# Kernel optimization log

Measured on AMD Instinct MI355X. Metric: run time of the kernel, lower is better.

## Reference

```python
import jax, jax.numpy as jnp
import numpy as np

B, S, F, E, H = 4, 2048, 512, 512, 8
DH = E // H


def setup_inputs() -> dict:
    key = jax.random.key(0)
    ks = jax.random.split(key, 8)
    sc = 1.0 / np.sqrt(F)
    return {
        "x": jax.random.normal(ks[0], (B, S, F), jnp.float32),
        "etype_emb": jax.random.normal(ks[1], (B, S, E), jnp.float32),
        "mask": jax.random.randint(ks[2], (B, S), 0, 2, jnp.int32),
        "Wq": jax.random.normal(ks[3], (F, E), jnp.float32) * sc,
        "bq": jnp.zeros((E,), jnp.float32),
        "Wk": jax.random.normal(ks[4], (F, E), jnp.float32) * sc,
        "bk": jnp.zeros((E,), jnp.float32),
        "Wv": jax.random.normal(ks[5], (F, E), jnp.float32) * sc,
        "bv": jnp.zeros((E,), jnp.float32),
    }


def _heads(t):
    # [B,S,E] -> [B,H,S,DH]; tf.split on last dim + concat on axis 1 == this reshape/transpose
    return t.reshape(B, S, H, DH).transpose(0, 2, 1, 3)


def reference(x, etype_emb, mask, Wq, bq, Wk, bk, Wv, bv):
    # Dropout is identity in inference mode (training=None)
    q = _heads(x @ Wq + bq + etype_emb)            # [B,H,S,DH]
    k = _heads(x @ Wk + bk)
    v = _heads(x @ Wv + bv)
    scores = jnp.einsum("bhqd,bhkd->bhqk", q, k) / jnp.sqrt(jnp.float32(DH))
    NEG = jnp.float32(-1e10)
    m = (mask == 1)
    # mask keys before softmax
    scores = jnp.where(m[:, None, None, :], scores, NEG)
    att = jax.nn.softmax(scores, axis=-1)
    # mask queries after softmax (zero out)
    att = jnp.where(m[:, None, :, None], att, jnp.float32(0.0))
    h = jnp.einsum("bhqk,bhkd->bhqd", att, v)       # [B,H,S,DH]
    return h.transpose(0, 2, 1, 3).reshape(B, S, E)
```

## Files before the change

### kernel.cpp

```cpp
#include <hip/hip_runtime.h>
#include <hip/hip_bf16.h>


typedef _Float16 f16x4 __attribute__((ext_vector_type(4)));
typedef _Float16 f16x8 __attribute__((ext_vector_type(8)));
typedef float f32x4 __attribute__((ext_vector_type(4)));

#define MFMA16(a, b, c) __builtin_amdgcn_mfma_f32_16x16x16f16((a), (b), (c), 0, 0, 0)
#define MFMA32(a, b, c) __builtin_amdgcn_mfma_f32_16x16x32_f16((a), (b), (c), 0, 0, 0)
#define GLDS16(g, l)                                                                     \
    __builtin_amdgcn_global_load_lds((const __attribute__((address_space(1))) void*)(g), \
                                     (__attribute__((address_space(3))) void*)(l), 16, 0, 0)

constexpr int Bn = 4, Sn = 2048, Fn = 512, En = 512, Hn = 8, DHn = 64;

__global__ void cvt_f32_to_f16(const float* __restrict__ in, _Float16* __restrict__ out, int n4) {
    int i = blockIdx.x * blockDim.x + threadIdx.x;
    int stride = gridDim.x * blockDim.x;
    for (; i < n4; i += stride) {
        float4 v = reinterpret_cast<const float4*>(in)[i];
        f16x4 o = { (_Float16)v.x, (_Float16)v.y, (_Float16)v.z, (_Float16)v.w };
        reinterpret_cast<f16x4*>(out)[i] = o;
    }
}

__global__ void cvt_wT(const float* __restrict__ Wq, const float* __restrict__ Wk,
                       const float* __restrict__ Wv, _Float16* __restrict__ out) {
    const int z = blockIdx.z;
    const float* W = (z == 0) ? Wq : ((z == 1) ? Wk : Wv);
    _Float16* o = out + (size_t)z * Fn * En;
    __shared__ float tile[16][17];
    int n = blockIdx.x * 16 + threadIdx.x;
    int k = blockIdx.y * 16 + threadIdx.y;
    tile[threadIdx.y][threadIdx.x] = W[k * En + n];
    __syncthreads();
    int n2 = blockIdx.x * 16 + threadIdx.y;
    int k2 = blockIdx.y * 16 + threadIdx.x;
    o[(size_t)n2 * Fn + k2] = (_Float16)tile[threadIdx.x][threadIdx.y];
}

__global__ __launch_bounds__(256, 6) void qkv_gemm(
    const _Float16* __restrict__ xh, const _Float16* __restrict__ wT,
    const float* __restrict__ bq, const float* __restrict__ bk, const float* __restrict__ bv,
    char* __restrict__ Qh, char* __restrict__ Kpk, char* __restrict__ Vpk) {
    const int z = blockIdx.z;
    const _Float16* Wz = wT + (size_t)z * Fn * En;
    const float* bias = (z == 0) ? bq : ((z == 1) ? bk : bv);

    const int tid = threadIdx.x;
    const int wave = tid >> 6, lane = tid & 63;
    const int lr = lane & 15, hi = lane >> 4;
    const int wr = wave >> 1, wn = wave & 1;
    const int m0 = blockIdx.x * 128;
    const int n0 = blockIdx.y * 64;

    __shared__ __align__(16) char smem[24576];
    char* As = smem;
    char* Bs = smem + 16384;

    f32x4 acc[4][2] = {};
    const int inrow = (tid & 7) * 16;
    const int rowb = tid >> 3;
    const char* xg = (const char*)xh;
    const char* wg = (const char*)Wz;

    for (int t = 0; t < 8; ++t) {
        const int k0b = t * 128;
        __syncthreads();
#pragma unroll
        for (int it = 0; it < 4; ++it) {
            const int row = rowb + it * 32;
            const int sc = inrow ^ ((row & 7) << 4);
            GLDS16(xg + (size_t)(m0 + row) * 1024 + k0b + sc, As + it * 4096 + tid * 16);
            if (it < 2)
                GLDS16(wg + (size_t)(n0 + row) * 1024 + k0b + sc, Bs + it * 4096 + tid * 16);
        }
        asm volatile("s_waitcnt vmcnt(0)" ::: "memory");
        __syncthreads();
#pragma unroll
        for (int ks = 0; ks < 2; ++ks) {
            const int kb = (ks * 64 + hi * 16) ^ ((lr & 7) << 4);
            f16x8 af[4], bf[2];
#pragma unroll
            for (int mt = 0; mt < 4; ++mt)
                af[mt] = *reinterpret_cast<const f16x8*>(As + (wr * 64 + mt * 16 + lr) * 128 + kb);
#pragma unroll
            for (int nt = 0; nt < 2; ++nt)
                bf[nt] = *reinterpret_cast<const f16x8*>(Bs + (wn * 32 + nt * 16 + lr) * 128 + kb);
#pragma unroll
            for (int mt = 0; mt < 4; ++mt)
#pragma unroll
                for (int nt = 0; nt < 2; ++nt)
                    acc[mt][nt] = MFMA32(af[mt], bf[nt], acc[mt][nt]);
        }
    }

    __syncthreads();
    {
        const int cb = wn * 32 + lr;
#pragma unroll
        for (int mt = 0; mt < 4; ++mt) {
            const int sb = wr * 64 + mt * 16 + hi * 4;
#pragma unroll
            for (int nt = 0; nt < 2; ++nt) {
                const int c = cb + nt * 16;
                const float bz = bias[n0 + c];
#pragma unroll
                for (int r = 0; r < 4; ++r) {
                    const int s = sb + r;
                    *reinterpret_cast<_Float16*>(smem + s * 128 + ((c * 2) ^ ((s & 7) << 4))) =
                        (_Float16)(acc[mt][nt][r] + bz);
                }
            }
        }
    }
    __syncthreads();

    const int bb = m0 >> 11;
    const int bh = bb * 8 + blockIdx.y;
    const int kt0 = (m0 & 2047) >> 6;
    char* outz = (z == 0) ? Qh : ((z == 1) ? Kpk : Vpk);
    char* hb = outz + (size_t)bh * 262144 + (size_t)kt0 * 8192;
    const char* sm = (const char*)smem;

#pragma unroll
    for (int j = 0; j < 4; ++j) {
        const int g = tid * 16 + j * 4096;
        const int T = g >> 13, g13 = g & 8191;
        f16x8 val;
        if (z == 0) {
            const int s = T * 64 + (g13 >> 7);
            val = *reinterpret_cast<const f16x8*>(sm + s * 128 + ((g13 & 127) ^ ((s & 7) << 4)));
        } else if (z == 1) {
            const int chunk = g13 >> 10, l2 = (g13 >> 4) & 63;
            const int s = T * 64 + (chunk >> 1) * 16 + (l2 & 15);
            const int db = (chunk & 1) * 64 + (l2 >> 4) * 16;
            val = *reinterpret_cast<const f16x8*>(sm + s * 128 + (db ^ ((s & 7) << 4)));
        } else {
            const int chunk = g13 >> 10, l2 = (g13 >> 4) & 63;
            const int ks = chunk >> 1, dp = chunk & 1;
            const int lr2 = l2 & 15, hi2 = l2 >> 4;
#pragma unroll
            for (int i = 0; i < 8; ++i) {
                const int d = (dp * 2 + (i >> 2)) * 16 + lr2;
                const int s = T * 64 + ks * 16 + hi2 * 4 + (i & 3);
                val[i] = *reinterpret_cast<const _Float16*>(sm + s * 128 + ((d * 2) ^ ((s & 7) << 4)));
            }
        }
        *reinterpret_cast<f16x8*>(hb + g) = val;
    }
}

__global__ __launch_bounds__(256, 4) void attn(
    const _Float16* __restrict__ Qh, const char* __restrict__ Kpk,
    const char* __restrict__ Vpk, const int* __restrict__ mask,
    const float* __restrict__ etype, float* __restrict__ out) {
    const int bid = blockIdx.x;
    const int bh = bid & 31, qb = bid >> 5;
    const int b = bh >> 3, h = bh & 7;
    const int tid = threadIdx.x;
    const int wave = tid >> 6, lane = tid & 63;
    const int lr = lane & 15, hi = lane >> 4;
    const int q0 = qb * 64 + wave * 16;

    const _Float16* Qb = Qh + (size_t)bh * Sn * DHn;
    const char* Kb = Kpk + (size_t)bh * 262144;
    const char* Vg = Vpk + (size_t)bh * 262144;
    const int* mb = mask + b * Sn;

    __shared__ __align__(16) char lds[40960];

    {
        const char* ms = (const char*)(mask + b * Sn);
        GLDS16(ms + tid * 16, lds + 32768 + tid * 16);
        GLDS16(ms + tid * 16 + 4096, lds + 32768 + tid * 16 + 4096);
        GLDS16(Kb + tid * 16, lds + tid * 16);
        GLDS16(Kb + tid * 16 + 4096, lds + tid * 16 + 4096);
        GLDS16(Vg + tid * 16, lds + 8192 + tid * 16);
        GLDS16(Vg + tid * 16 + 4096, lds + 8192 + tid * 16 + 4096);
    }

    constexpr float CSC = 0.18033688011112042f;
    f16x8 qf[2];
#pragma unroll
    for (int ks = 0; ks < 2; ++ks) {
        const f16x8 qh = *reinterpret_cast<const f16x8*>(Qb + (q0 + lr) * DHn + ks * 32 + hi * 8);
        const float* ep = etype + ((size_t)(b * Sn) + q0 + lr) * En + h * DHn + ks * 32 + hi * 8;
        const f32x4 e0 = *reinterpret_cast<const f32x4*>(ep);
        const f32x4 e1 = *reinterpret_cast<const f32x4*>(ep + 4);
        f16x8 q;
#pragma unroll
        for (int j = 0; j < 4; ++j) q[j] = (_Float16)(((float)qh[j] + e0[j]) * CSC);
#pragma unroll
        for (int j = 0; j < 4; ++j) q[4 + j] = (_Float16)(((float)qh[4 + j] + e1[j]) * CSC);
        qf[ks] = q;
    }

    f32x4 oaccT[4] = {};
    f32x4 osum = {};
    float mrun = -3e38f;
    const f16x4 onev = {(_Float16)1.f, (_Float16)1.f, (_Float16)1.f, (_Float16)1.f};

    asm volatile("s_waitcnt vmcnt(0)" ::: "memory");
    __syncthreads();

    {
        int4 a = *reinterpret_cast<const int4*>(lds + 32768 + tid * 16);
        int4 c = *reinterpret_cast<const int4*>(lds + 32768 + tid * 16 + 4096);
        __syncthreads();
        f32x4 fa = {a.x ? 0.f : -1e30f, a.y ? 0.f : -1e30f, a.z ? 0.f : -1e30f, a.w ? 0.f : -1e30f};
        f32x4 fc = {c.x ? 0.f : -1e30f, c.y ? 0.f : -1e30f, c.z ? 0.f : -1e30f, c.w ? 0.f : -1e30f};
        *reinterpret_cast<f32x4*>(lds + 32768 + tid * 16) = fa;
        *reinterpret_cast<f32x4*>(lds + 32768 + tid * 16 + 4096) = fc;
        __syncthreads();
    }

    const char* kvr = lds + lane * 16;
    const char* pmb = lds + 32768 + hi * 16;

    for (int tp = 0; tp < 16; ++tp) {
        const int tb = tp * 512;
#pragma unroll
        for (int u = 0; u < 2; ++u) {
            const int t = tp * 2 + u;
            const size_t nto = (size_t)((t + 1) & 31) * 8192;
            char* nb = lds + (u ^ 1) * 16384;
            GLDS16(Kb + nto + tid * 16, nb + tid * 16);
            GLDS16(Kb + nto + tid * 16 + 4096, nb + tid * 16 + 4096);
            GLDS16(Vg + nto + tid * 16, nb + 8192 + tid * 16);
            GLDS16(Vg + nto + tid * 16 + 4096, nb + 8192 + tid * 16 + 4096);

            f32x4 scT[4];
#pragma unroll
            for (int kt = 0; kt < 4; ++kt)
                scT[kt] = *reinterpret_cast<const f32x4*>(pmb + tb + u * 256 + kt * 64);

            const char* cb = kvr + u * 16384;
#pragma unroll
            for (int ks = 0; ks < 2; ++ks)
#pragma unroll
                for (int kt = 0; kt < 4; ++kt) {
                    const f16x8 kf = *reinterpret_cast<const f16x8*>(cb + (kt * 2 + ks) * 1024);
                    scT[kt] = MFMA32(kf, qf[ks], scT[kt]);
                }

            float mx = fmaxf(fmaxf(scT[0][0], scT[0][1]), fmaxf(scT[0][2], scT[0][3]));
            mx = fmaxf(mx, fmaxf(fmaxf(scT[1][0], scT[1][1]), fmaxf(scT[1][2], scT[1][3])));
            mx = fmaxf(mx, fmaxf(fmaxf(scT[2][0], scT[2][1]), fmaxf(scT[2][2], scT[2][3])));
            mx = fmaxf(mx, fmaxf(fmaxf(scT[3][0], scT[3][1]), fmaxf(scT[3][2], scT[3][3])));
            mx = fmaxf(mx, __shfl_xor(mx, 16));
            mx = fmaxf(mx, __shfl_xor(mx, 32));

            if (!__all(mx <= mrun + 8.0f)) {
                const float mnew = fmaxf(mrun, mx);
                const float al = exp2f(mrun - mnew);
                mrun = mnew;
#pragma unroll
                for (int dt = 0; dt < 4; ++dt) oaccT[dt] *= al;
                osum *= al;
            }

            f16x4 pa[4];
#pragma unroll
            for (int kt = 0; kt < 4; ++kt) {
                f16x4 p;
#pragma unroll
                for (int r = 0; r < 4; ++r) p[r] = (_Float16)exp2f(scT[kt][r] - mrun);
                pa[kt] = p;
            }

#pragma unroll
            for (int ks = 0; ks < 4; ++ks) {
#pragma unroll
                for (int dp = 0; dp < 2; ++dp) {
                    const f16x8 vv = *reinterpret_cast<const f16x8*>(cb + 8192 + (ks * 2 + dp) * 1024);
                    const f16x4 v0 = {vv[0], vv[1], vv[2], vv[3]};
                    const f16x4 v1 = {vv[4], vv[5], vv[6], vv[7]};
                    oaccT[dp * 2] = MFMA16(v0, pa[ks], oaccT[dp * 2]);
                    oaccT[dp * 2 + 1] = MFMA16(v1, pa[ks], oaccT[dp * 2 + 1]);
                }
                osum = MFMA16(onev, pa[ks], osum);
            }

            asm volatile("s_waitcnt vmcnt(0)" ::: "memory");
            __syncthreads();
        }
    }

    const int srow = q0 + lr;
    const float inv = (mb[srow] != 0) ? 1.0f / osum[0] : 0.0f;
#pragma unroll
    for (int dt = 0; dt < 4; ++dt) {
        f32x4 o = oaccT[dt] * inv;
        *reinterpret_cast<f32x4*>(out + ((size_t)(b * Sn + srow)) * En + h * DHn + dt * 16 + hi * 4) = o;
    }
}

extern "C" void kernel_launch(void* const* d_in, const int* in_sizes, int n_in,
                              void* d_out, int out_size, void* d_ws, size_t ws_size,
                              hipStream_t stream) {
    const float* x = (const float*)d_in[0];
    const float* etype = (const float*)d_in[1];
    const int* mask = (const int*)d_in[2];
    const float* Wq = (const float*)d_in[3];
    const float* bq = (const float*)d_in[4];
    const float* Wk = (const float*)d_in[5];
    const float* bk = (const float*)d_in[6];
    const float* Wv = (const float*)d_in[7];
    const float* bv = (const float*)d_in[8];
    float* out = (float*)d_out;

    char* ws = (char*)d_ws;
    _Float16* xh = (_Float16*)(ws + 0);
    _Float16* wT = (_Float16*)(ws + 8388608);
    char* Qh = ws + 9961472;
    char* Kpk = ws + 18350080;
    char* Vpk = ws + 26738688;

    cvt_f32_to_f16<<<2048, 256, 0, stream>>>(x, xh, (Bn * Sn * Fn) / 4);
    cvt_wT<<<dim3(32, 32, 3), dim3(16, 16), 0, stream>>>(Wq, Wk, Wv, wT);
    qkv_gemm<<<dim3(64, 8, 3), 256, 0, stream>>>(xh, wT, bq, bk, bv, Qh, Kpk, Vpk);
    attn<<<1024, 256, 0, stream>>>((const _Float16*)Qh, Kpk, Vpk, mask, etype, out);
}
```

Before: 189.9 us.

## Double-buffer QKV GEMM LDS tiles and remap blocks for L2 locality

The QKV projection GEMM now double-buffers its LDS tiles, issuing the global-to-LDS loads for the next K step before computing on the current one, so memory latency can overlap the MFMA work. The grid is flattened to 1D and block indices are remapped so groups of 8 adjacent M-tiles run together across all z/y outputs, which is meant to improve L2 reuse of x rows. LDS use doubles to 48KB and launch bounds drop to 3 blocks per CU, which may reduce occupancy. The last iteration issues a redundant prefetch of tile 0 that is never used.

```diff
diff --git a/kernel.cpp b/kernel.cpp
--- a/kernel.cpp
+++ b/kernel.cpp
@@ -39,11 +39,16 @@
     o[(size_t)n2 * Fn + k2] = (_Float16)tile[threadIdx.x][threadIdx.y];
 }
 
-__global__ __launch_bounds__(256, 6) void qkv_gemm(
+__global__ __launch_bounds__(256, 3) void qkv_gemm(
     const _Float16* __restrict__ xh, const _Float16* __restrict__ wT,
     const float* __restrict__ bq, const float* __restrict__ bk, const float* __restrict__ bv,
     char* __restrict__ Qh, char* __restrict__ Kpk, char* __restrict__ Vpk) {
-    const int z = blockIdx.z;
+    const int hwbid = blockIdx.x;
+    const int t2 = hwbid >> 3;
+    const int x = (t2 / 24) * 8 + (hwbid & 7);
+    const int r = t2 % 24;
+    const int z = r >> 3, y = r & 7;
+
     const _Float16* Wz = wT + (size_t)z * Fn * En;
     const float* bias = (z == 0) ? bq : ((z == 1) ? bk : bv);
 
@@ -51,12 +56,10 @@
     const int wave = tid >> 6, lane = tid & 63;
     const int lr = lane & 15, hi = lane >> 4;
     const int wr = wave >> 1, wn = wave & 1;
-    const int m0 = blockIdx.x * 128;
-    const int n0 = blockIdx.y * 64;
-
-    __shared__ __align__(16) char smem[24576];
-    char* As = smem;
-    char* Bs = smem + 16384;
+    const int m0 = x * 128;
+    const int n0 = y * 64;
+
+    __shared__ __align__(16) char smem[49152];
 
     f32x4 acc[4][2] = {};
     const int inrow = (tid & 7) * 16;
@@ -64,38 +67,53 @@
     const char* xg = (const char*)xh;
     const char* wg = (const char*)Wz;
 
-    for (int t = 0; t < 8; ++t) {
+    auto stage = [&](int t, char* dst) {
         const int k0b = t * 128;
-        __syncthreads();
 #pragma unroll
         for (int it = 0; it < 4; ++it) {
             const int row = rowb + it * 32;
             const int sc = inrow ^ ((row & 7) << 4);
-            GLDS16(xg + (size_t)(m0 + row) * 1024 + k0b + sc, As + it * 4096 + tid * 16);
+            GLDS16(xg + (size_t)(m0 + row) * 1024 + k0b + sc, dst + it * 4096 + tid * 16);
             if (it < 2)
-                GLDS16(wg + (size_t)(n0 + row) * 1024 + k0b + sc, Bs + it * 4096 + tid * 16);
-        }
-        asm volatile("s_waitcnt vmcnt(0)" ::: "memory");
-        __syncthreads();
-#pragma unroll
-        for (int ks = 0; ks < 2; ++ks) {
-            const int kb = (ks * 64 + hi * 16) ^ ((lr & 7) << 4);
-            f16x8 af[4], bf[2];
-#pragma unroll
-            for (int mt = 0; mt < 4; ++mt)
-                af[mt] = *reinterpret_cast<const f16x8*>(As + (wr * 64 + mt * 16 + lr) * 128 + kb);
-#pragma unroll
-            for (int nt = 0; nt < 2; ++nt)
-                bf[nt] = *reinterpret_cast<const f16x8*>(Bs + (wn * 32 + nt * 16 + lr) * 128 + kb);
-#pragma unroll
-            for (int mt = 0; mt < 4; ++mt)
+                GLDS16(wg + (size_t)(n0 + row) * 1024 + k0b + sc, dst + 16384 + it * 4096 + tid * 16);
+        }
+    };
+
+    stage(0, smem);
+    asm volatile("s_waitcnt vmcnt(0)" ::: "memory");
+    __syncthreads();
+
+    for (int tp = 0; tp < 4; ++tp) {
+#pragma unroll
+        for (int u = 0; u < 2; ++u) {
+            const int t = tp * 2 + u;
+            char* cur = smem + u * 24576;
+            char* nxt = smem + (u ^ 1) * 24576;
+            stage((t + 1) & 7, nxt);
+
+            char* As = cur;
+            char* Bs = cur + 16384;
+#pragma unroll
+            for (int ks = 0; ks < 2; ++ks) {
+                const int kb = (ks * 64 + hi * 16) ^ ((lr & 7) << 4);
+                f16x8 af[4], bf[2];
+#pragma unroll
+                for (int mt = 0; mt < 4; ++mt)
+                    af[mt] = *reinterpret_cast<const f16x8*>(As + (wr * 64 + mt * 16 + lr) * 128 + kb);
 #pragma unroll
                 for (int nt = 0; nt < 2; ++nt)
-                    acc[mt][nt] = MFMA32(af[mt], bf[nt], acc[mt][nt]);
-        }
-    }
-
-    __syncthreads();
+                    bf[nt] = *reinterpret_cast<const f16x8*>(Bs + (wn * 32 + nt * 16 + lr) * 128 + kb);
+#pragma unroll
+                for (int mt = 0; mt < 4; ++mt)
+#pragma unroll
+                    for (int nt = 0; nt < 2; ++nt)
+                        acc[mt][nt] = MFMA32(af[mt], bf[nt], acc[mt][nt]);
+            }
+            asm volatile("s_waitcnt vmcnt(0)" ::: "memory");
+            __syncthreads();
+        }
+    }
+
     {
         const int cb = wn * 32 + lr;
 #pragma unroll
@@ -106,10 +124,10 @@
                 const int c = cb + nt * 16;
                 const float bz = bias[n0 + c];
 #pragma unroll
-                for (int r = 0; r < 4; ++r) {
-                    const int s = sb + r;
+                for (int r2 = 0; r2 < 4; ++r2) {
+                    const int s = sb + r2;
                     *reinterpret_cast<_Float16*>(smem + s * 128 + ((c * 2) ^ ((s & 7) << 4))) =
-                        (_Float16)(acc[mt][nt][r] + bz);
+                        (_Float16)(acc[mt][nt][r2] + bz);
                 }
             }
         }
@@ -117,7 +135,7 @@
     __syncthreads();
 
     const int bb = m0 >> 11;
-    const int bh = bb * 8 + blockIdx.y;
+    const int bh = bb * 8 + y;
     const int kt0 = (m0 & 2047) >> 6;
     char* outz = (z == 0) ? Qh : ((z == 1) ? Kpk : Vpk);
     char* hb = outz + (size_t)bh * 262144 + (size_t)kt0 * 8192;
@@ -319,6 +337,6 @@
 
     cvt_f32_to_f16<<<2048, 256, 0, stream>>>(x, xh, (Bn * Sn * Fn) / 4);
     cvt_wT<<<dim3(32, 32, 3), dim3(16, 16), 0, stream>>>(Wq, Wk, Wv, wT);
-    qkv_gemm<<<dim3(64, 8, 3), 256, 0, stream>>>(xh, wT, bq, bk, bv, Qh, Kpk, Vpk);
+    qkv_gemm<<<1536, 256, 0, stream>>>(xh, wT, bq, bk, bv, Qh, Kpk, Vpk);
     attn<<<1024, 256, 0, stream>>>((const _Float16*)Qh, Kpk, Vpk, mask, etype, out);
 }
```

Result: faster. 181.4 us (-4.5%).
